# Kernel tuning notes

Hardware: AMD Instinct MI355X
Metric: run time of the kernel (lower is better)

## Reference

```python
import jax, jax.numpy as jnp
import numpy as np

B, S, D, H, F, REF = 4, 1024, 512, 8, 2048, 2
HGRID = 32   # sqrt(seq_len)
HALF = 3     # 7x7 window -> half-width 3


def _masks():
    i = jnp.arange(HGRID)
    near = jnp.abs(i[:, None] - i[None, :]) <= HALF            # [h,h]
    inside = (near[:, None, :, None] & near[None, :, None, :]).reshape(S, S)
    # reverse=True mask (mca): outside-window -> -inf, inside -> 0
    m_rev = jnp.where(inside, 0.0, -jnp.inf).astype(jnp.float32)
    # reverse=False mask (msa/nsa): inside-window -> -inf, outside -> 0 (faithful to source)
    m_fwd = jnp.where(inside, -jnp.inf, 0.0).astype(jnp.float32)
    return m_rev, m_fwd


def _mha(q, k, v, w, b, ow, ob, mask):
    # torch nn.MultiheadAttention, batch_first, eval mode (no dropout)
    hd = D // H
    wq, wk, wv = jnp.split(w, 3, axis=0)
    bq, bk, bv = jnp.split(b, 3)

    def proj(t, wt, bt):
        Bt, Lt = t.shape[0], t.shape[1]
        return (t @ wt.T + bt).reshape(Bt, Lt, H, hd).transpose(0, 2, 1, 3)

    qh, kh, vh = proj(q, wq, bq), proj(k, wk, bk), proj(v, wv, bv)
    scores = jnp.einsum('bhqd,bhkd->bhqk', qh, kh) / jnp.sqrt(jnp.float32(hd))
    if mask is not None:
        scores = scores + mask
    a = jax.nn.softmax(scores, axis=-1)
    o = jnp.einsum('bhqk,bhkd->bhqd', a, vh).transpose(0, 2, 1, 3).reshape(q.shape[0], q.shape[1], D)
    return o @ ow.T + ob


def _ln(x, g, b, eps=1e-5):
    m = x.mean(-1, keepdims=True)
    v = ((x - m) ** 2).mean(-1, keepdims=True)
    return (x - m) / jnp.sqrt(v + eps) * g + b


def setup_inputs() -> dict:
    key = jax.random.key(0)
    ks = jax.random.split(key, 16)
    d = {}
    d['x'] = jax.random.normal(ks[0], (B, S, D), jnp.float32)
    d['ref_mca'] = jax.random.normal(ks[1], (B, REF * S, D), jnp.float32)
    d['gate'] = jax.random.uniform(ks[2], (B, S, 5), jnp.float32)
    i = 3
    for p in ['mca', 'ca', 'msa', 'nsa', 'sa']:
        d[p + '_w'] = 0.02 * jax.random.normal(ks[i], (3 * D, D), jnp.float32); i += 1
        d[p + '_b'] = jnp.zeros((3 * D,), jnp.float32)
        d[p + '_ow'] = 0.02 * jax.random.normal(ks[i], (D, D), jnp.float32); i += 1
        d[p + '_ob'] = jnp.zeros((D,), jnp.float32)
    d['ln1_g'] = jnp.ones((D,), jnp.float32); d['ln1_b'] = jnp.zeros((D,), jnp.float32)
    d['ln2_g'] = jnp.ones((D,), jnp.float32); d['ln2_b'] = jnp.zeros((D,), jnp.float32)
    d['fc1_w'] = 0.02 * jax.random.normal(ks[i], (F, D), jnp.float32); i += 1
    d['fc1_b'] = jnp.zeros((F,), jnp.float32)
    d['fc2_w'] = 0.02 * jax.random.normal(ks[i], (D, F), jnp.float32); i += 1
    d['fc2_b'] = jnp.zeros((D,), jnp.float32)
    return d


def reference(x, ref_mca, gate,
              mca_w, mca_b, mca_ow, mca_ob,
              ca_w, ca_b, ca_ow, ca_ob,
              msa_w, msa_b, msa_ow, msa_ob,
              nsa_w, nsa_b, nsa_ow, nsa_ob,
              sa_w, sa_b, sa_ow, sa_ob,
              ln1_g, ln1_b, ln2_g, ln2_b,
              fc1_w, fc1_b, fc2_w, fc2_b):
    m_rev, m_fwd = _masks()
    # mca branch: sum attention over each seq_len chunk of ref_mca (window-inside mask)
    mca_x = jnp.zeros_like(x)
    for r in range(REF):
        chunk = ref_mca[:, r * S:(r + 1) * S, :]
        mca_x = mca_x + _mha(x, chunk, chunk, mca_w, mca_b, mca_ow, mca_ob, m_rev)
    # faithful to source: loop variable leaks, so ca/nsa use the LAST chunk
    ref_last = ref_mca[:, (REF - 1) * S:, :]
    new_x = gate[:, :, 0:1] * mca_x
    new_x = new_x + gate[:, :, 1:2] * _mha(x, ref_last, ref_last, ca_w, ca_b, ca_ow, ca_ob, None)
    new_x = new_x + gate[:, :, 2:3] * _mha(x, x, x, msa_w, msa_b, msa_ow, msa_ob, m_fwd)
    new_x = new_x + gate[:, :, 3:4] * _mha(x, ref_last, x, nsa_w, nsa_b, nsa_ow, nsa_ob, m_fwd)
    new_x = new_x + gate[:, :, 4:5] * _mha(x, x, x, sa_w, sa_b, sa_ow, sa_ob, None)
    h = _ln(new_x, ln1_g, ln1_b)
    y = jax.nn.gelu(h @ fc1_w.T + fc1_b, approximate=False) @ fc2_w.T + fc2_b
    return _ln(h + y, ln2_g, ln2_b)
```

## Files before the change

kernel.cpp:

```cpp
#include <hip/hip_runtime.h>

typedef __bf16 bf16_t;
typedef bf16_t bf16x8 __attribute__((ext_vector_type(8)));
typedef float f32x4v __attribute__((ext_vector_type(4)));
typedef unsigned int u32;

__device__ __forceinline__ void gload16(const bf16_t* g, bf16_t* l) {
    __builtin_amdgcn_global_load_lds((const __attribute__((address_space(1))) u32*)g,
                                     (__attribute__((address_space(3))) u32*)l, 16, 0, 0);
}

struct PackBDesc {
    int nseg;
    int blkOf[21];
    const float* src[20];
    bf16_t* dst[20];
    int chunks[20];
    int dstLd[20];
    int shift[20];
};

__global__ __launch_bounds__(256) void packb_k(PackBDesc d) {
    int b = blockIdx.x;
    int s = 0;
    while (s + 1 < d.nseg && b >= d.blkOf[s + 1]) ++s;
    int idx = (b - d.blkOf[s]) * 256 + threadIdx.x;
    if (idx >= d.chunks[s]) return;
    const float* src = d.src[s] + (size_t)idx * 8;
    int r = idx >> d.shift[s];
    int c8 = idx & ((1 << d.shift[s]) - 1);
    bf16_t* dst = d.dst[s] + (size_t)r * d.dstLd[s] + (size_t)c8 * 8;
    float4 v0 = reinterpret_cast<const float4*>(src)[0];
    float4 v1 = reinterpret_cast<const float4*>(src)[1];
    bf16x8 o;
    o[0] = (bf16_t)v0.x; o[1] = (bf16_t)v0.y; o[2] = (bf16_t)v0.z; o[3] = (bf16_t)v0.w;
    o[4] = (bf16_t)v1.x; o[5] = (bf16_t)v1.y; o[6] = (bf16_t)v1.z; o[7] = (bf16_t)v1.w;
    *reinterpret_cast<bf16x8*>(dst) = o;
}

struct PackFDesc {
    int nseg;
    int blkOf[15];
    const float* src[14];
    float* dst[14];
    int n[14];
};

__global__ __launch_bounds__(256) void packf_k(PackFDesc d) {
    int b = blockIdx.x;
    int s = 0;
    while (s + 1 < d.nseg && b >= d.blkOf[s + 1]) ++s;
    int idx = (b - d.blkOf[s]) * 256 + threadIdx.x;
    if (idx >= d.n[s]) return;
    d.dst[s][idx] = d.src[s][idx];
}

template <int EPI, int BM, int BN>
__device__ __forceinline__ void gemm_core(
    int tm, int tn, int bz,
    const bf16_t* __restrict__ A, int aBS, int aRowOff, int lda,
    const bf16_t* __restrict__ B,
    const float* __restrict__ bias,
    void* __restrict__ Out, int ldo, size_t outSplitStride,
    const float* __restrict__ gate, const float* __restrict__ obcat,
    int kStart, int kLen) {
    constexpr int MB = BM / 32, NB = BN / 32, WM = BM / 2, WN = BN / 2;
    constexpr int CA = BM / 64, CB = BN / 64;
    __shared__ __attribute__((aligned(16))) bf16_t As[2][BM * 32];
    __shared__ __attribute__((aligned(16))) bf16_t Bs[2][BN * 32];
    const int tid = threadIdx.x, lane = tid & 63, w = tid >> 6;
    const int wm = w >> 1, wn = w & 1;
    const int l15 = lane & 15, l16 = lane >> 4;
    const int colS = (lane & 3) * 8, rowS = lane >> 2;

    auto remap = [&](int m) { return (m >> 10) * aBS + aRowOff + (m & 1023); };

    const bf16_t* aS[CA];
    const bf16_t* bS[CB];
#pragma unroll
    for (int c = 0; c < CA; ++c)
        aS[c] = A + (size_t)remap(tm * BM + (CA * w + c) * 16 + rowS) * lda + kStart + colS;
#pragma unroll
    for (int c = 0; c < CB; ++c)
        bS[c] = B + (size_t)(tn * BN + (CB * w + c) * 16 + rowS) * lda + kStart + colS;

    auto stage = [&](int buf, int t) {
        const size_t o = (size_t)t * 32;
#pragma unroll
        for (int c = 0; c < CA; ++c) gload16(aS[c] + o, &As[buf][(CA * w + c) * 512]);
#pragma unroll
        for (int c = 0; c < CB; ++c) gload16(bS[c] + o, &Bs[buf][(CB * w + c) * 512]);
    };

    f32x4v acc[MB][NB] = {};
    const int nt = kLen / 32;
    stage(0, 0);
    __syncthreads();
    int cur = 0;
    for (int t = 0; t < nt; ++t) {
        if (t + 1 < nt) stage(cur ^ 1, t + 1);
        bf16x8 af[MB], bff[NB];
#pragma unroll
        for (int mi = 0; mi < MB; ++mi)
            af[mi] = *reinterpret_cast<const bf16x8*>(&As[cur][(wm * WM + mi * 16 + l15) * 32 + l16 * 8]);
#pragma unroll
        for (int ni = 0; ni < NB; ++ni)
            bff[ni] = *reinterpret_cast<const bf16x8*>(&Bs[cur][(wn * WN + ni * 16 + l15) * 32 + l16 * 8]);
#pragma unroll
        for (int mi = 0; mi < MB; ++mi)
#pragma unroll
            for (int ni = 0; ni < NB; ++ni)
                acc[mi][ni] = __builtin_amdgcn_mfma_f32_16x16x32_bf16(af[mi], bff[ni], acc[mi][ni], 0, 0, 0);
        __syncthreads();
        cur ^= 1;
    }

#pragma unroll
    for (int mi = 0; mi < MB; ++mi) {
#pragma unroll
        for (int ni = 0; ni < NB; ++ni) {
#pragma unroll
            for (int i = 0; i < 4; ++i) {
                int row = tm * BM + wm * WM + mi * 16 + l16 * 4 + i;
                int n = tn * BN + wn * WN + ni * 16 + l15;
                float v = acc[mi][ni][i];
                if (bias && bz == 0) v += bias[n];
                if constexpr (EPI == 0) {
                    ((bf16_t*)Out)[(size_t)row * ldo + n] = (bf16_t)v;
                } else if constexpr (EPI == 1) {
                    float g = 0.5f * v * (1.0f + erff(v * 0.70710678118654752f));
                    ((bf16_t*)Out)[(size_t)row * ldo + n] = (bf16_t)g;
                } else if constexpr (EPI == 3) {
                    ((float*)Out + (size_t)bz * outSplitStride)[(size_t)row * ldo + n] = v;
                } else {
                    if (obcat && bz == 0) {
#pragma unroll
                        for (int p = 0; p < 5; ++p) {
                            float c = (p == 0) ? 2.0f : 1.0f;
                            v += gate[row * 5 + p] * c * obcat[p * 512 + n];
                        }
                    }
                    ((float*)Out + (size_t)bz * outSplitStride)[(size_t)row * ldo + n] = v;
                }
            }
        }
    }
}

struct ProjDesc {
    const bf16_t* A[3];
    int aBS[3], aRowOff[3];
    const bf16_t* B[3];
    const float* bias[3];
    bf16_t* Out[3];
    int ldo[3];
    int ntn[3], base[3];
};

__global__ __launch_bounds__(256) void proj_k(ProjDesc d) {
    int bx = blockIdx.x;
    int s = (bx >= d.base[2]) ? 2 : (bx >= d.base[1]) ? 1 : 0;
    int local = bx - d.base[s];
    int tn = local % d.ntn[s];
    int tm = local / d.ntn[s];
    gemm_core<0, 128, 64>(tm, tn, 0, d.A[s], d.aBS[s], d.aRowOff[s], 512,
                          d.B[s], d.bias[s], d.Out[s], d.ldo[s], 0, nullptr, nullptr, 0, 512);
}

template <int EPI, int BM, int BN>
__global__ __launch_bounds__(256) void gemmT(
    const bf16_t* __restrict__ A, int aBS, int aRowOff, int lda,
    const bf16_t* __restrict__ B, const float* __restrict__ bias,
    void* __restrict__ Out, int ldo, size_t outSplitStride,
    const float* __restrict__ gate, const float* __restrict__ obcat, int kPerSplit) {
    gemm_core<EPI, BM, BN>(blockIdx.y, blockIdx.x, blockIdx.z, A, aBS, aRowOff, lda, B, bias,
                           Out, ldo, outSplitStride, gate, obcat, blockIdx.z * kPerSplit, kPerSplit);
}

struct AttnDesc {
    const bf16_t* Q[6];
    const bf16_t* K[6];
    const bf16_t* V[6];
    int ldq[6], ldk[6], ldv[6];
    int segOff[6], gidx[6], mask[6];
    bf16_t* acat;
    bf16_t* Op;
    float* Mp;
    float* Lp;
    const float* gate;
};

__global__ __launch_bounds__(256) void attn4_k(AttnDesc d) {
    __shared__ __attribute__((aligned(16))) bf16_t Ks[32][72];
    __shared__ __attribute__((aligned(16))) bf16_t Vt[64][40];
    __shared__ __attribute__((aligned(16))) bf16_t Ps[4][16][40];

    int bx = blockIdx.x;
    int u, local;
    if (bx < 512) { u = 0; local = bx; }
    else if (bx < 1024) { u = 1; local = bx - 512; }
    else if (bx < 2048) { u = 2; local = bx - 1024; }
    else if (bx < 3072) { u = 3; local = bx - 2048; }
    else if (bx < 4096) { u = 4; local = bx - 3072; }
    else { u = 5; local = bx - 4096; }
    const bool splitk = (u >= 2);
    const int mask = d.mask[u];
    const int qt = local & 15, h = (local >> 4) & 7, z = local >> 7;

    const int tid = threadIdx.x;
    const int lane = tid & 63;
    const int w = tid >> 6;
    const int l15 = lane & 15, l16 = lane >> 4;

    int b, split;
    if (splitk) { b = z & 3; split = z >> 2; } else { b = z; split = 0; }

    const int qr = qt * 64 + w * 16;
    const int qrow = b * 1024 + qr;
    const int qblk = qr >> 5;
    const int qg = ((w & 1) * 16) + l15;

    const bf16_t* Q = d.Q[u];
    const int ldq = d.ldq[u], ldk = d.ldk[u], ldv = d.ldv[u];

    bf16x8 aq[2];
#pragma unroll
    for (int s = 0; s < 2; ++s)
        aq[s] = *reinterpret_cast<const bf16x8*>(
            Q + (size_t)(qrow + l15) * ldq + h * 64 + s * 32 + l16 * 8);

    float mrow = -1e30f, lsum = 0.f;
    f32x4v accO[4] = {};

    const int srow = tid >> 3, scol8 = (tid & 7) * 8;
    const bf16_t* kbase = d.K[u] + (size_t)(b * 1024) * ldk + h * 64 + scol8;
    const bf16_t* vbase = d.V[u] + (size_t)(b * 1024) * ldv + h * 64 + scol8;

    int kt0, ktEnd;
    if (splitk) { kt0 = split * 16; ktEnd = kt0 + 16; }
    else {
        int qb0 = qt * 2;
        kt0 = qb0 - 3; if (kt0 < 0) kt0 = 0;
        ktEnd = qb0 + 5; if (ktEnd > 32) ktEnd = 32;
    }

    bf16x8 rk, rv, rk2, rv2;
    rk = *reinterpret_cast<const bf16x8*>(kbase + (size_t)(kt0 * 32 + srow) * ldk);
    rv = *reinterpret_cast<const bf16x8*>(vbase + (size_t)(kt0 * 32 + srow) * ldv);

    for (int kt = kt0; kt < ktEnd; ++kt) {
        __syncthreads();
        *reinterpret_cast<bf16x8*>(&Ks[srow][scol8]) = rk;
#pragma unroll
        for (int j = 0; j < 8; ++j) {
            int dd = scol8 + j;
            Vt[dd][srow ^ (((dd >> 3) & 3) << 3)] = rv[j];
        }
        if (kt + 1 < ktEnd) {
            rk2 = *reinterpret_cast<const bf16x8*>(kbase + (size_t)((kt + 1) * 32 + srow) * ldk);
            rv2 = *reinterpret_cast<const bf16x8*>(vbase + (size_t)((kt + 1) * 32 + srow) * ldv);
        }
        __syncthreads();

        int bd = qblk - kt; if (bd < 0) bd = -bd;
        const bool active = (mask != 1) || (bd <= 3);
        if (active) {
            bf16x8 k00 = *reinterpret_cast<const bf16x8*>(&Ks[l15][l16 * 8]);
            bf16x8 k01 = *reinterpret_cast<const bf16x8*>(&Ks[l15][32 + l16 * 8]);
            bf16x8 k10 = *reinterpret_cast<const bf16x8*>(&Ks[16 + l15][l16 * 8]);
            bf16x8 k11 = *reinterpret_cast<const bf16x8*>(&Ks[16 + l15][32 + l16 * 8]);
            f32x4v z0 = {}, z1 = {};
            z0 = __builtin_amdgcn_mfma_f32_16x16x32_bf16(k00, aq[0], z0, 0, 0, 0);
            z0 = __builtin_amdgcn_mfma_f32_16x16x32_bf16(k01, aq[1], z0, 0, 0, 0);
            z1 = __builtin_amdgcn_mfma_f32_16x16x32_bf16(k10, aq[0], z1, 0, 0, 0);
            z1 = __builtin_amdgcn_mfma_f32_16x16x32_bf16(k11, aq[1], z1, 0, 0, 0);

            const bool needMask = (mask == 1) || (mask == 2 && bd <= 3);
            float p[2][4];
#pragma unroll
            for (int n = 0; n < 2; ++n) {
                f32x4v sv = n ? z1 : z0;
#pragma unroll
                for (int i = 0; i < 4; ++i) {
                    float v = sv[i] * 0.125f;
                    if (needMask) {
                        int k5 = n * 16 + l16 * 4 + i;
                        int dq = qg - k5; if (dq < 0) dq = -dq;
                        bool inside = (dq <= 3);
                        if (mask == 1 ? !inside : inside) v = -1e30f;
                    }
                    p[n][i] = v;
                }
            }
            float tmx = p[0][0];
            tmx = fmaxf(tmx, p[0][1]); tmx = fmaxf(tmx, p[0][2]); tmx = fmaxf(tmx, p[0][3]);
            tmx = fmaxf(tmx, p[1][0]); tmx = fmaxf(tmx, p[1][1]);
            tmx = fmaxf(tmx, p[1][2]); tmx = fmaxf(tmx, p[1][3]);
            tmx = fmaxf(tmx, __shfl_xor(tmx, 16, 64));
            tmx = fmaxf(tmx, __shfl_xor(tmx, 32, 64));
            float mn = fmaxf(mrow, tmx);
            float fac = __expf(mrow - mn);
            mrow = mn;
            float rs = 0.f;
#pragma unroll
            for (int n = 0; n < 2; ++n)
#pragma unroll
                for (int i = 0; i < 4; ++i) {
                    p[n][i] = __expf(p[n][i] - mn);
                    rs += p[n][i];
                }
            rs += __shfl_xor(rs, 16, 64);
            rs += __shfl_xor(rs, 32, 64);
            lsum = lsum * fac + rs;

            float facq[4];
#pragma unroll
            for (int i = 0; i < 4; ++i) facq[i] = __shfl(fac, l16 * 4 + i, 64);
#pragma unroll
            for (int dblk = 0; dblk < 4; ++dblk)
#pragma unroll
                for (int i = 0; i < 4; ++i) accO[dblk][i] *= facq[i];

#pragma unroll
            for (int n = 0; n < 2; ++n)
#pragma unroll
                for (int i = 0; i < 4; ++i)
                    Ps[w][l15][n * 16 + l16 * 4 + i] = (bf16_t)p[n][i];
            bf16x8 pa = *reinterpret_cast<const bf16x8*>(&Ps[w][l15][l16 * 8]);

#pragma unroll
            for (int dblk = 0; dblk < 4; ++dblk) {
                int dd = dblk * 16 + l15;
                bf16x8 bv = *reinterpret_cast<const bf16x8*>(&Vt[dd][(l16 ^ ((dd >> 3) & 3)) * 8]);
                accO[dblk] = __builtin_amdgcn_mfma_f32_16x16x32_bf16(pa, bv, accO[dblk], 0, 0, 0);
            }
        }
        rk = rk2; rv = rv2;
    }

    if (!splitk) {
        float inv = 1.0f / lsum;
        float invq[4];
#pragma unroll
        for (int i = 0; i < 4; ++i) invq[i] = __shfl(inv, l16 * 4 + i, 64);
#pragma unroll
        for (int dblk = 0; dblk < 4; ++dblk)
#pragma unroll
            for (int i = 0; i < 4; ++i) {
                float g = d.gate[(size_t)(qrow + l16 * 4 + i) * 5 + d.gidx[u]];
                d.acat[(size_t)(qrow + l16 * 4 + i) * 3072 + d.segOff[u] + h * 64 + dblk * 16 + l15] =
                    (bf16_t)(accO[dblk][i] * invq[i] * g);
            }
    } else {
        const int su = u - 2;
        bf16_t* Opu = d.Op + (size_t)su * 65536 * 64;
        float* Mpu = d.Mp + su * 65536;
        float* Lpu = d.Lp + su * 65536;
        int pb = ((split * 4 + b) * 8 + h) * 1024 + qr;
        if (l16 == 0) { Mpu[pb + l15] = mrow; Lpu[pb + l15] = lsum; }
#pragma unroll
        for (int dblk = 0; dblk < 4; ++dblk)
#pragma unroll
            for (int i = 0; i < 4; ++i) {
                float g = d.gate[(size_t)(qrow + l16 * 4 + i) * 5 + d.gidx[u]];
                Opu[(size_t)(pb + l16 * 4 + i) * 64 + dblk * 16 + l15] = (bf16_t)(accO[dblk][i] * g);
            }
    }
}

struct MergeDesc {
    const bf16_t* Op;
    const float* Mp;
    const float* Lp;
    bf16_t* acat;
    int segOff[4];
};

__global__ __launch_bounds__(256) void merge4_k(MergeDesc d) {
    int u = blockIdx.x >> 10;
    int idx = (blockIdx.x & 1023) * 256 + threadIdx.x;
    const bf16_t* Opu = d.Op + (size_t)u * 65536 * 64;
    const float* Mpu = d.Mp + u * 65536;
    const float* Lpu = d.Lp + u * 65536;
    int dg = idx & 7;
    int q = (idx >> 3) & 1023;
    int h = (idx >> 13) & 7;
    int b = idx >> 16;
    int r0 = ((0 * 4 + b) * 8 + h) * 1024 + q;
    int r1 = ((1 * 4 + b) * 8 + h) * 1024 + q;
    float m0 = Mpu[r0], m1 = Mpu[r1], l0 = Lpu[r0], l1 = Lpu[r1];
    float M = fmaxf(m0, m1);
    float w0 = __expf(m0 - M), w1 = __expf(m1 - M);
    float den = 1.0f / (l0 * w0 + l1 * w1);
    bf16x8 o0 = *reinterpret_cast<const bf16x8*>(Opu + (size_t)r0 * 64 + dg * 8);
    bf16x8 o1 = *reinterpret_cast<const bf16x8*>(Opu + (size_t)r1 * 64 + dg * 8);
    bf16x8 o;
#pragma unroll
    for (int j = 0; j < 8; ++j)
        o[j] = (bf16_t)(((float)o0[j] * w0 + (float)o1[j] * w1) * den);
    *reinterpret_cast<bf16x8*>(d.acat + (size_t)(b * 1024 + q) * 3072 + d.segOff[u] + h * 64 + dg * 8) = o;
}

__global__ __launch_bounds__(256) void ln_k(const float* __restrict__ in0,
                                            const float* __restrict__ in1,
                                            const float* __restrict__ in2,
                                            const float* __restrict__ g,
                                            const float* __restrict__ bb,
                                            float* __restrict__ outf,
                                            bf16_t* __restrict__ outb) {
    __shared__ float red[8];
    int row = blockIdx.x;
    int t = threadIdx.x;
    float x0 = in0[(size_t)row * 512 + t];
    float x1 = in0[(size_t)row * 512 + 256 + t];
    if (in1) {
        x0 += in1[(size_t)row * 512 + t];
        x1 += in1[(size_t)row * 512 + 256 + t];
    }
    if (in2) {
        x0 += in2[(size_t)row * 512 + t];
        x1 += in2[(size_t)row * 512 + 256 + t];
    }
    float s = x0 + x1, sq = x0 * x0 + x1 * x1;
#pragma unroll
    for (int d = 1; d < 64; d <<= 1) {
        s += __shfl_xor(s, d, 64);
        sq += __shfl_xor(sq, d, 64);
    }
    int w = t >> 6;
    if ((t & 63) == 0) { red[w] = s; red[4 + w] = sq; }
    __syncthreads();
    s = red[0] + red[1] + red[2] + red[3];
    sq = red[4] + red[5] + red[6] + red[7];
    float mean = s * (1.0f / 512.0f);
    float var = sq * (1.0f / 512.0f) - mean * mean;
    float rstd = rsqrtf(var + 1e-5f);
    float y0 = (x0 - mean) * rstd * g[t] + bb[t];
    float y1 = (x1 - mean) * rstd * g[256 + t] + bb[256 + t];
    if (outf) {
        outf[(size_t)row * 512 + t] = y0;
        outf[(size_t)row * 512 + 256 + t] = y1;
    }
    if (outb) {
        outb[(size_t)row * 512 + t] = (bf16_t)y0;
        outb[(size_t)row * 512 + 256 + t] = (bf16_t)y1;
    }
}

extern "C" void kernel_launch(void* const* d_in, const int* in_sizes, int n_in,
                              void* d_out, int out_size, void* d_ws, size_t ws_size,
                              hipStream_t stream) {
    (void)in_sizes; (void)n_in; (void)out_size; (void)ws_size;
    const float* x       = (const float*)d_in[0];
    const float* ref_mca = (const float*)d_in[1];
    const float* gate    = (const float*)d_in[2];
    const float *w[5], *wb[5], *ow[5], *ob[5];
    for (int p = 0; p < 5; ++p) {
        w[p]  = (const float*)d_in[3 + p * 4];
        wb[p] = (const float*)d_in[4 + p * 4];
        ow[p] = (const float*)d_in[5 + p * 4];
        ob[p] = (const float*)d_in[6 + p * 4];
    }
    const float* ln1_g = (const float*)d_in[23];
    const float* ln1_b = (const float*)d_in[24];
    const float* ln2_g = (const float*)d_in[25];
    const float* ln2_b = (const float*)d_in[26];
    const float* fc1_w = (const float*)d_in[27];
    const float* fc1_b = (const float*)d_in[28];
    const float* fc2_w = (const float*)d_in[29];
    const float* fc2_b = (const float*)d_in[30];

    char* ws = (char*)d_ws;
    size_t off = 0;
    auto alloc = [&](size_t bytes) {
        char* p = ws + off;
        off += (bytes + 255) & ~(size_t)255;
        return p;
    };
    const size_t S2 = (size_t)4096 * 512;
    bf16_t* xb    = (bf16_t*)alloc(S2 * 2);
    bf16_t* refb  = (bf16_t*)alloc((size_t)8192 * 512 * 2);
    bf16_t* Wxp   = (bf16_t*)alloc((size_t)5120 * 512 * 2);
    bf16_t* WRp   = (bf16_t*)alloc((size_t)2560 * 512 * 2);
    bf16_t* Wop   = (bf16_t*)alloc((size_t)512 * 3072 * 2);
    bf16_t* fc1p  = (bf16_t*)alloc((size_t)2048 * 512 * 2);
    bf16_t* fc2p  = (bf16_t*)alloc((size_t)512 * 2048 * 2);
    float*  bxp   = (float*)alloc((size_t)5120 * 4);
    float*  brp   = (float*)alloc((size_t)2560 * 4);
    float*  obc   = (float*)alloc((size_t)5 * 512 * 4);
    bf16_t* XP    = (bf16_t*)alloc((size_t)4096 * 5120 * 2);
    bf16_t* RP    = (bf16_t*)alloc((size_t)4096 * 2560 * 2);
    bf16_t* R0    = (bf16_t*)alloc((size_t)4096 * 1024 * 2);
    bf16_t* acat  = (bf16_t*)alloc((size_t)4096 * 3072 * 2);
    float*  newx  = (float*)alloc(S2 * 4 * 2);
    float*  hbuf  = (float*)alloc(S2 * 4);
    bf16_t* Opart = (bf16_t*)alloc((size_t)4 * 65536 * 64 * 2);
    float*  Mpart = (float*)alloc((size_t)4 * 65536 * 4);
    float*  Lpart = (float*)alloc((size_t)4 * 65536 * 4);
    bf16_t* hb  = refb;
    bf16_t* ub  = XP;
    float*  yp  = newx;

    PackBDesc pb{};
    int nb = 0, blk = 0;
    auto addB = [&](const float* s, bf16_t* dptr, int chunks, int dstLd, int shift) {
        pb.src[nb] = s; pb.dst[nb] = dptr; pb.chunks[nb] = chunks;
        pb.dstLd[nb] = dstLd; pb.shift[nb] = shift;
        pb.blkOf[nb] = blk; blk += (chunks + 255) / 256; ++nb;
    };
    auto addLin = [&](const float* s, bf16_t* dptr, long elems) {
        addB(s, dptr, (int)(elems / 8), 0, 30);
    };
    addLin(x, xb, (long)4096 * 512);
    addLin(ref_mca, refb, (long)8192 * 512);
    addLin(w[0], Wxp, (long)512 * 512);
    addLin(w[1], Wxp + (size_t)512 * 512, (long)512 * 512);
    addLin(w[2], Wxp + (size_t)1024 * 512, (long)1536 * 512);
    addLin(w[3], Wxp + (size_t)2560 * 512, (long)512 * 512);
    addLin(w[3] + (size_t)1024 * 512, Wxp + (size_t)3072 * 512, (long)512 * 512);
    addLin(w[4], Wxp + (size_t)3584 * 512, (long)1536 * 512);
    addLin(w[0] + (size_t)512 * 512, WRp, (long)1024 * 512);
    addLin(w[1] + (size_t)512 * 512, WRp + (size_t)1024 * 512, (long)1024 * 512);
    addLin(w[3] + (size_t)512 * 512, WRp + (size_t)2048 * 512, (long)512 * 512);
    const float* owSeg[6] = {ow[0], ow[0], ow[1], ow[2], ow[3], ow[4]};
    for (int s = 0; s < 6; ++s)
        addB(owSeg[s], Wop + (size_t)s * 512, 32768, 3072, 6);
    addLin(fc1_w, fc1p, (long)2048 * 512);
    addLin(fc2_w, fc2p, (long)512 * 2048);
    pb.nseg = nb; pb.blkOf[nb] = blk;
    packb_k<<<blk, 256, 0, stream>>>(pb);

    PackFDesc pf{};
    int nf = 0, fblk = 0;
    auto addF = [&](const float* s, float* dptr, int n) {
        pf.src[nf] = s; pf.dst[nf] = dptr; pf.n[nf] = n;
        pf.blkOf[nf] = fblk; fblk += (n + 255) / 256; ++nf;
    };
    addF(wb[0], bxp, 512);
    addF(wb[1], bxp + 512, 512);
    addF(wb[2], bxp + 1024, 1536);
    addF(wb[3], bxp + 2560, 512);
    addF(wb[3] + 1024, bxp + 3072, 512);
    addF(wb[4], bxp + 3584, 1536);
    addF(wb[0] + 512, brp, 1024);
    addF(wb[1] + 512, brp + 1024, 1024);
    addF(wb[3] + 512, brp + 2048, 512);
    for (int p = 0; p < 5; ++p) addF(ob[p], obc + p * 512, 512);
    pf.nseg = nf; pf.blkOf[nf] = fblk;
    packf_k<<<fblk, 256, 0, stream>>>(pf);

    ProjDesc pd{};
    pd.A[0] = xb;   pd.aBS[0] = 1024; pd.aRowOff[0] = 0;    pd.B[0] = Wxp; pd.bias[0] = bxp; pd.Out[0] = XP; pd.ldo[0] = 5120; pd.ntn[0] = 80;
    pd.A[1] = refb; pd.aBS[1] = 2048; pd.aRowOff[1] = 1024; pd.B[1] = WRp; pd.bias[1] = brp; pd.Out[1] = RP; pd.ldo[1] = 2560; pd.ntn[1] = 40;
    pd.A[2] = refb; pd.aBS[2] = 2048; pd.aRowOff[2] = 0;    pd.B[2] = WRp; pd.bias[2] = brp; pd.Out[2] = R0; pd.ldo[2] = 1024; pd.ntn[2] = 16;
    pd.base[0] = 0; pd.base[1] = 80 * 32; pd.base[2] = 80 * 32 + 40 * 32;
    proj_k<<<80 * 32 + 40 * 32 + 16 * 32, 256, 0, stream>>>(pd);

    AttnDesc ad{};
    auto setU = [&](int u, const bf16_t* Q, int lq, const bf16_t* K, int lk,
                    const bf16_t* V, int lv, int seg, int gi, int mk) {
        ad.Q[u] = Q; ad.ldq[u] = lq; ad.K[u] = K; ad.ldk[u] = lk; ad.V[u] = V; ad.ldv[u] = lv;
        ad.segOff[u] = seg; ad.gidx[u] = gi; ad.mask[u] = mk;
    };
    setU(0, XP, 5120, R0, 1024, R0 + 512, 1024, 0, 0, 1);
    setU(1, XP, 5120, RP, 2560, RP + 512, 2560, 512, 0, 1);
    setU(2, XP + 512, 5120, RP + 1024, 2560, RP + 1536, 2560, 1024, 1, 0);
    setU(3, XP + 1024, 5120, XP + 1536, 5120, XP + 2048, 5120, 1536, 2, 2);
    setU(4, XP + 2560, 5120, RP + 2048, 2560, XP + 3072, 5120, 2048, 3, 2);
    setU(5, XP + 3584, 5120, XP + 4096, 5120, XP + 4608, 5120, 2560, 4, 0);
    ad.acat = acat; ad.Op = Opart; ad.Mp = Mpart; ad.Lp = Lpart; ad.gate = gate;
    attn4_k<<<5120, 256, 0, stream>>>(ad);

    MergeDesc md{};
    md.Op = Opart; md.Mp = Mpart; md.Lp = Lpart; md.acat = acat;
    md.segOff[0] = 1024; md.segOff[1] = 1536; md.segOff[2] = 2048; md.segOff[3] = 2560;
    merge4_k<<<4096, 256, 0, stream>>>(md);

    gemmT<4, 64, 64><<<dim3(8, 64, 2), 256, 0, stream>>>(acat, 1024, 0, 3072, Wop, nullptr,
                                                         newx, 512, S2, gate, obc, 1536);
    ln_k<<<4096, 256, 0, stream>>>(newx, newx + S2, nullptr, ln1_g, ln1_b, hbuf, hb);
    gemmT<1, 64, 128><<<dim3(16, 64, 1), 256, 0, stream>>>(hb, 1024, 0, 512, fc1p, fc1_b,
                                                           ub, 2048, 0, nullptr, nullptr, 512);
    gemmT<3, 64, 64><<<dim3(8, 64, 2), 256, 0, stream>>>(ub, 1024, 0, 2048, fc2p, fc2_b,
                                                         yp, 512, S2, nullptr, nullptr, 1024);
    ln_k<<<4096, 256, 0, stream>>>(hbuf, yp, yp + S2, ln2_g, ln2_b, (float*)d_out, nullptr);
}
```

Baseline: 315.6 us.

## Enlarge attention tiles to 128 queries x 64 keys with XCD-aware block ordering

The attention kernel now runs 512-thread blocks, each covering 128 query rows and 64-key tiles. This halves the block count and K/V reload traffic per query and doubles reuse of each shared-memory tile. Blocks are remapped so heads and units interleave across the 8 XCDs, and masking handles the two 32-key halves of each tile separately. The projection and FC1 GEMMs move to 128x128 tiles, and the projection grid is XCD-swizzled. The costs are higher shared-memory and register use per block and fewer blocks, which can lower occupancy. The hardcoded 272 stride in the swizzle depends on the grid size.

```diff
diff --git a/kernel.cpp b/kernel.cpp
--- a/kernel.cpp
+++ b/kernel.cpp
@@ -158,13 +158,13 @@
 };
 
 __global__ __launch_bounds__(256) void proj_k(ProjDesc d) {
-    int bx = blockIdx.x;
-    int s = (bx >= d.base[2]) ? 2 : (bx >= d.base[1]) ? 1 : 0;
-    int local = bx - d.base[s];
+    int wg = (blockIdx.x & 7) * 272 + (blockIdx.x >> 3);
+    int s = (wg >= d.base[2]) ? 2 : (wg >= d.base[1]) ? 1 : 0;
+    int local = wg - d.base[s];
     int tn = local % d.ntn[s];
     int tm = local / d.ntn[s];
-    gemm_core<0, 128, 64>(tm, tn, 0, d.A[s], d.aBS[s], d.aRowOff[s], 512,
-                          d.B[s], d.bias[s], d.Out[s], d.ldo[s], 0, nullptr, nullptr, 0, 512);
+    gemm_core<0, 128, 128>(tm, tn, 0, d.A[s], d.aBS[s], d.aRowOff[s], 512,
+                           d.B[s], d.bias[s], d.Out[s], d.ldo[s], 0, nullptr, nullptr, 0, 512);
 }
 
 template <int EPI, int BM, int BN>
@@ -190,112 +190,116 @@
     const float* gate;
 };
 
-__global__ __launch_bounds__(256) void attn4_k(AttnDesc d) {
-    __shared__ __attribute__((aligned(16))) bf16_t Ks[32][72];
-    __shared__ __attribute__((aligned(16))) bf16_t Vt[64][40];
-    __shared__ __attribute__((aligned(16))) bf16_t Ps[4][16][40];
-
-    int bx = blockIdx.x;
-    int u, local;
-    if (bx < 512) { u = 0; local = bx; }
-    else if (bx < 1024) { u = 1; local = bx - 512; }
-    else if (bx < 2048) { u = 2; local = bx - 1024; }
-    else if (bx < 3072) { u = 3; local = bx - 2048; }
-    else if (bx < 4096) { u = 4; local = bx - 3072; }
-    else { u = 5; local = bx - 4096; }
+__global__ __launch_bounds__(512) void attn5_k(AttnDesc d) {
+    __shared__ __attribute__((aligned(16))) bf16_t Ks[64][72];
+    __shared__ __attribute__((aligned(16))) bf16_t Vt[64][72];
+    __shared__ __attribute__((aligned(16))) bf16_t Ps[8][16][40];
+
+    int bid = blockIdx.x;
+    int xcd = bid & 7;
+    int t = bid >> 3;
+    int qt = t / 40;
+    int g = (t % 40) * 8 + xcd;
+    int u, lg;
+    if (g < 32) { u = 0; lg = g; }
+    else if (g < 64) { u = 1; lg = g - 32; }
+    else if (g < 128) { u = 2; lg = g - 64; }
+    else if (g < 192) { u = 3; lg = g - 128; }
+    else if (g < 256) { u = 4; lg = g - 192; }
+    else { u = 5; lg = g - 256; }
     const bool splitk = (u >= 2);
     const int mask = d.mask[u];
-    const int qt = local & 15, h = (local >> 4) & 7, z = local >> 7;
+    const int h = lg & 7, z = lg >> 3;
+    int b, split;
+    if (splitk) { b = z & 3; split = z >> 2; } else { b = z; split = 0; }
 
     const int tid = threadIdx.x;
     const int lane = tid & 63;
     const int w = tid >> 6;
     const int l15 = lane & 15, l16 = lane >> 4;
 
-    int b, split;
-    if (splitk) { b = z & 3; split = z >> 2; } else { b = z; split = 0; }
-
-    const int qr = qt * 64 + w * 16;
+    const int qr = qt * 128 + w * 16;
     const int qrow = b * 1024 + qr;
     const int qblk = qr >> 5;
     const int qg = ((w & 1) * 16) + l15;
 
-    const bf16_t* Q = d.Q[u];
     const int ldq = d.ldq[u], ldk = d.ldk[u], ldv = d.ldv[u];
-
     bf16x8 aq[2];
 #pragma unroll
     for (int s = 0; s < 2; ++s)
         aq[s] = *reinterpret_cast<const bf16x8*>(
-            Q + (size_t)(qrow + l15) * ldq + h * 64 + s * 32 + l16 * 8);
+            d.Q[u] + (size_t)(qrow + l15) * ldq + h * 64 + s * 32 + l16 * 8);
 
     float mrow = -1e30f, lsum = 0.f;
     f32x4v accO[4] = {};
 
     const int srow = tid >> 3, scol8 = (tid & 7) * 8;
+    const int vcol = srow ^ ((tid & 7) << 3);
     const bf16_t* kbase = d.K[u] + (size_t)(b * 1024) * ldk + h * 64 + scol8;
     const bf16_t* vbase = d.V[u] + (size_t)(b * 1024) * ldv + h * 64 + scol8;
 
-    int kt0, ktEnd;
-    if (splitk) { kt0 = split * 16; ktEnd = kt0 + 16; }
+    int t0, t1;
+    if (splitk) { t0 = split * 8; t1 = t0 + 8; }
     else {
-        int qb0 = qt * 2;
-        kt0 = qb0 - 3; if (kt0 < 0) kt0 = 0;
-        ktEnd = qb0 + 5; if (ktEnd > 32) ktEnd = 32;
+        int klo = qt * 4 - 3; if (klo < 0) klo = 0;
+        int khi = qt * 4 + 6; if (khi > 31) khi = 31;
+        t0 = klo >> 1; t1 = (khi >> 1) + 1;
     }
 
     bf16x8 rk, rv, rk2, rv2;
-    rk = *reinterpret_cast<const bf16x8*>(kbase + (size_t)(kt0 * 32 + srow) * ldk);
-    rv = *reinterpret_cast<const bf16x8*>(vbase + (size_t)(kt0 * 32 + srow) * ldv);
-
-    for (int kt = kt0; kt < ktEnd; ++kt) {
+    rk = *reinterpret_cast<const bf16x8*>(kbase + (size_t)(t0 * 64 + srow) * ldk);
+    rv = *reinterpret_cast<const bf16x8*>(vbase + (size_t)(t0 * 64 + srow) * ldv);
+
+    for (int tt = t0; tt < t1; ++tt) {
         __syncthreads();
         *reinterpret_cast<bf16x8*>(&Ks[srow][scol8]) = rk;
 #pragma unroll
-        for (int j = 0; j < 8; ++j) {
-            int dd = scol8 + j;
-            Vt[dd][srow ^ (((dd >> 3) & 3) << 3)] = rv[j];
-        }
-        if (kt + 1 < ktEnd) {
-            rk2 = *reinterpret_cast<const bf16x8*>(kbase + (size_t)((kt + 1) * 32 + srow) * ldk);
-            rv2 = *reinterpret_cast<const bf16x8*>(vbase + (size_t)((kt + 1) * 32 + srow) * ldv);
+        for (int j = 0; j < 8; ++j) Vt[scol8 + j][vcol] = rv[j];
+        if (tt + 1 < t1) {
+            rk2 = *reinterpret_cast<const bf16x8*>(kbase + (size_t)((tt + 1) * 64 + srow) * ldk);
+            rv2 = *reinterpret_cast<const bf16x8*>(vbase + (size_t)((tt + 1) * 64 + srow) * ldv);
         }
         __syncthreads();
 
-        int bd = qblk - kt; if (bd < 0) bd = -bd;
-        const bool active = (mask != 1) || (bd <= 3);
-        if (active) {
-            bf16x8 k00 = *reinterpret_cast<const bf16x8*>(&Ks[l15][l16 * 8]);
-            bf16x8 k01 = *reinterpret_cast<const bf16x8*>(&Ks[l15][32 + l16 * 8]);
-            bf16x8 k10 = *reinterpret_cast<const bf16x8*>(&Ks[16 + l15][l16 * 8]);
-            bf16x8 k11 = *reinterpret_cast<const bf16x8*>(&Ks[16 + l15][32 + l16 * 8]);
-            f32x4v z0 = {}, z1 = {};
-            z0 = __builtin_amdgcn_mfma_f32_16x16x32_bf16(k00, aq[0], z0, 0, 0, 0);
-            z0 = __builtin_amdgcn_mfma_f32_16x16x32_bf16(k01, aq[1], z0, 0, 0, 0);
-            z1 = __builtin_amdgcn_mfma_f32_16x16x32_bf16(k10, aq[0], z1, 0, 0, 0);
-            z1 = __builtin_amdgcn_mfma_f32_16x16x32_bf16(k11, aq[1], z1, 0, 0, 0);
-
-            const bool needMask = (mask == 1) || (mask == 2 && bd <= 3);
-            float p[2][4];
-#pragma unroll
-            for (int n = 0; n < 2; ++n) {
-                f32x4v sv = n ? z1 : z0;
+        int bd0 = qblk - tt * 2;     if (bd0 < 0) bd0 = -bd0;
+        int bd1 = qblk - tt * 2 - 1; if (bd1 < 0) bd1 = -bd1;
+        const bool a0 = (mask != 1) || (bd0 <= 3);
+        const bool a1 = (mask != 1) || (bd1 <= 3);
+        if (a0 || a1) {
+            f32x4v z4[4];
+#pragma unroll
+            for (int nt = 0; nt < 4; ++nt) {
+                bf16x8 kf0 = *reinterpret_cast<const bf16x8*>(&Ks[nt * 16 + l15][l16 * 8]);
+                bf16x8 kf1 = *reinterpret_cast<const bf16x8*>(&Ks[nt * 16 + l15][32 + l16 * 8]);
+                f32x4v zz = {};
+                zz = __builtin_amdgcn_mfma_f32_16x16x32_bf16(kf0, aq[0], zz, 0, 0, 0);
+                zz = __builtin_amdgcn_mfma_f32_16x16x32_bf16(kf1, aq[1], zz, 0, 0, 0);
+                z4[nt] = zz;
+            }
+            float p[4][4];
+#pragma unroll
+            for (int nt = 0; nt < 4; ++nt) {
+                const int bd = (nt >> 1) ? bd1 : bd0;
+                const bool act = (nt >> 1) ? a1 : a0;
+                const bool needMask = (mask == 1) || (mask == 2 && bd <= 3);
 #pragma unroll
                 for (int i = 0; i < 4; ++i) {
-                    float v = sv[i] * 0.125f;
-                    if (needMask) {
-                        int k5 = n * 16 + l16 * 4 + i;
+                    float v = z4[nt][i] * 0.125f;
+                    if (!act) v = -1e30f;
+                    else if (needMask) {
+                        int k5 = (nt & 1) * 16 + l16 * 4 + i;
                         int dq = qg - k5; if (dq < 0) dq = -dq;
-                        bool inside = (dq <= 3);
+                        bool inside = (bd <= 3) && (dq <= 3);
                         if (mask == 1 ? !inside : inside) v = -1e30f;
                     }
-                    p[n][i] = v;
+                    p[nt][i] = v;
                 }
             }
             float tmx = p[0][0];
-            tmx = fmaxf(tmx, p[0][1]); tmx = fmaxf(tmx, p[0][2]); tmx = fmaxf(tmx, p[0][3]);
-            tmx = fmaxf(tmx, p[1][0]); tmx = fmaxf(tmx, p[1][1]);
-            tmx = fmaxf(tmx, p[1][2]); tmx = fmaxf(tmx, p[1][3]);
+#pragma unroll
+            for (int nt = 0; nt < 4; ++nt)
+#pragma unroll
+                for (int i = 0; i < 4; ++i) tmx = fmaxf(tmx, p[nt][i]);
             tmx = fmaxf(tmx, __shfl_xor(tmx, 16, 64));
             tmx = fmaxf(tmx, __shfl_xor(tmx, 32, 64));
             float mn = fmaxf(mrow, tmx);
@@ -303,11 +307,11 @@
             mrow = mn;
             float rs = 0.f;
 #pragma unroll
-            for (int n = 0; n < 2; ++n)
+            for (int nt = 0; nt < 4; ++nt)
 #pragma unroll
                 for (int i = 0; i < 4; ++i) {
-                    p[n][i] = __expf(p[n][i] - mn);
-                    rs += p[n][i];
+                    p[nt][i] = __expf(p[nt][i] - mn);
+                    rs += p[nt][i];
                 }
             rs += __shfl_xor(rs, 16, 64);
             rs += __shfl_xor(rs, 32, 64);
@@ -322,17 +326,20 @@
                 for (int i = 0; i < 4; ++i) accO[dblk][i] *= facq[i];
 
 #pragma unroll
-            for (int n = 0; n < 2; ++n)
-#pragma unroll
-                for (int i = 0; i < 4; ++i)
-                    Ps[w][l15][n * 16 + l16 * 4 + i] = (bf16_t)p[n][i];
-            bf16x8 pa = *reinterpret_cast<const bf16x8*>(&Ps[w][l15][l16 * 8]);
-
-#pragma unroll
-            for (int dblk = 0; dblk < 4; ++dblk) {
-                int dd = dblk * 16 + l15;
-                bf16x8 bv = *reinterpret_cast<const bf16x8*>(&Vt[dd][(l16 ^ ((dd >> 3) & 3)) * 8]);
-                accO[dblk] = __builtin_amdgcn_mfma_f32_16x16x32_bf16(pa, bv, accO[dblk], 0, 0, 0);
+            for (int kh = 0; kh < 2; ++kh) {
+#pragma unroll
+                for (int n = 0; n < 2; ++n)
+#pragma unroll
+                    for (int i = 0; i < 4; ++i)
+                        Ps[w][l15][n * 16 + l16 * 4 + i] = (bf16_t)p[kh * 2 + n][i];
+                bf16x8 pa = *reinterpret_cast<const bf16x8*>(&Ps[w][l15][l16 * 8]);
+#pragma unroll
+                for (int dblk = 0; dblk < 4; ++dblk) {
+                    int dd = dblk * 16 + l15;
+                    int csw = ((kh * 4 + l16) ^ (dd >> 3)) * 8;
+                    bf16x8 bv = *reinterpret_cast<const bf16x8*>(&Vt[dd][csw]);
+                    accO[dblk] = __builtin_amdgcn_mfma_f32_16x16x32_bf16(pa, bv, accO[dblk], 0, 0, 0);
+                }
             }
         }
         rk = rk2; rv = rv2;
@@ -347,9 +354,9 @@
         for (int dblk = 0; dblk < 4; ++dblk)
 #pragma unroll
             for (int i = 0; i < 4; ++i) {
-                float g = d.gate[(size_t)(qrow + l16 * 4 + i) * 5 + d.gidx[u]];
+                float gg = d.gate[(size_t)(qrow + l16 * 4 + i) * 5 + d.gidx[u]];
                 d.acat[(size_t)(qrow + l16 * 4 + i) * 3072 + d.segOff[u] + h * 64 + dblk * 16 + l15] =
-                    (bf16_t)(accO[dblk][i] * invq[i] * g);
+                    (bf16_t)(accO[dblk][i] * invq[i] * gg);
             }
     } else {
         const int su = u - 2;
@@ -362,8 +369,8 @@
         for (int dblk = 0; dblk < 4; ++dblk)
 #pragma unroll
             for (int i = 0; i < 4; ++i) {
-                float g = d.gate[(size_t)(qrow + l16 * 4 + i) * 5 + d.gidx[u]];
-                Opu[(size_t)(pb + l16 * 4 + i) * 64 + dblk * 16 + l15] = (bf16_t)(accO[dblk][i] * g);
+                float gg = d.gate[(size_t)(qrow + l16 * 4 + i) * 5 + d.gidx[u]];
+                Opu[(size_t)(pb + l16 * 4 + i) * 64 + dblk * 16 + l15] = (bf16_t)(accO[dblk][i] * gg);
             }
     }
 }
@@ -550,11 +557,11 @@
     packf_k<<<fblk, 256, 0, stream>>>(pf);
 
     ProjDesc pd{};
-    pd.A[0] = xb;   pd.aBS[0] = 1024; pd.aRowOff[0] = 0;    pd.B[0] = Wxp; pd.bias[0] = bxp; pd.Out[0] = XP; pd.ldo[0] = 5120; pd.ntn[0] = 80;
-    pd.A[1] = refb; pd.aBS[1] = 2048; pd.aRowOff[1] = 1024; pd.B[1] = WRp; pd.bias[1] = brp; pd.Out[1] = RP; pd.ldo[1] = 2560; pd.ntn[1] = 40;
-    pd.A[2] = refb; pd.aBS[2] = 2048; pd.aRowOff[2] = 0;    pd.B[2] = WRp; pd.bias[2] = brp; pd.Out[2] = R0; pd.ldo[2] = 1024; pd.ntn[2] = 16;
-    pd.base[0] = 0; pd.base[1] = 80 * 32; pd.base[2] = 80 * 32 + 40 * 32;
-    proj_k<<<80 * 32 + 40 * 32 + 16 * 32, 256, 0, stream>>>(pd);
+    pd.A[0] = xb;   pd.aBS[0] = 1024; pd.aRowOff[0] = 0;    pd.B[0] = Wxp; pd.bias[0] = bxp; pd.Out[0] = XP; pd.ldo[0] = 5120; pd.ntn[0] = 40;
+    pd.A[1] = refb; pd.aBS[1] = 2048; pd.aRowOff[1] = 1024; pd.B[1] = WRp; pd.bias[1] = brp; pd.Out[1] = RP; pd.ldo[1] = 2560; pd.ntn[1] = 20;
+    pd.A[2] = refb; pd.aBS[2] = 2048; pd.aRowOff[2] = 0;    pd.B[2] = WRp; pd.bias[2] = brp; pd.Out[2] = R0; pd.ldo[2] = 1024; pd.ntn[2] = 8;
+    pd.base[0] = 0; pd.base[1] = 40 * 32; pd.base[2] = 40 * 32 + 20 * 32;
+    proj_k<<<(40 + 20 + 8) * 32, 256, 0, stream>>>(pd);
 
     AttnDesc ad{};
     auto setU = [&](int u, const bf16_t* Q, int lq, const bf16_t* K, int lk,
@@ -569,7 +576,7 @@
     setU(4, XP + 2560, 5120, RP + 2048, 2560, XP + 3072, 5120, 2048, 3, 2);
     setU(5, XP + 3584, 5120, XP + 4096, 5120, XP + 4608, 5120, 2560, 4, 0);
     ad.acat = acat; ad.Op = Opart; ad.Mp = Mpart; ad.Lp = Lpart; ad.gate = gate;
-    attn4_k<<<5120, 256, 0, stream>>>(ad);
+    attn5_k<<<2560, 512, 0, stream>>>(ad);
 
     MergeDesc md{};
     md.Op = Opart; md.Mp = Mpart; md.Lp = Lpart; md.acat = acat;
@@ -579,8 +586,8 @@
     gemmT<4, 64, 64><<<dim3(8, 64, 2), 256, 0, stream>>>(acat, 1024, 0, 3072, Wop, nullptr,
                                                          newx, 512, S2, gate, obc, 1536);
     ln_k<<<4096, 256, 0, stream>>>(newx, newx + S2, nullptr, ln1_g, ln1_b, hbuf, hb);
-    gemmT<1, 64, 128><<<dim3(16, 64, 1), 256, 0, stream>>>(hb, 1024, 0, 512, fc1p, fc1_b,
-                                                           ub, 2048, 0, nullptr, nullptr, 512);
+    gemmT<1, 128, 128><<<dim3(16, 32, 1), 256, 0, stream>>>(hb, 1024, 0, 512, fc1p, fc1_b,
+                                                            ub, 2048, 0, nullptr, nullptr, 512);
     gemmT<3, 64, 64><<<dim3(8, 64, 2), 256, 0, stream>>>(ub, 1024, 0, 2048, fc2p, fc2_b,
                                                          yp, 512, S2, nullptr, nullptr, 1024);
     ln_k<<<4096, 256, 0, stream>>>(hbuf, yp, yp + S2, ln2_g, ln2_b, (float*)d_out, nullptr);
```

Result: slower. 324.9 us (+3.0%).
